# Optimization experiments

Hardware: AMD Instinct MI355X
Metric: run time of the kernel (lower is better)

Reference implementation:

```python
import jax, jax.numpy as jnp
import numpy as np

N_NODES = 100000
N_EDGES = 500000
HEADS = 4
HID = 64
N_GRAPHS = 512
EPS_SM = 1e-8
EPS_BN = 1e-5


def setup_inputs() -> dict:
    key = jax.random.key(0)
    ks = jax.random.split(key, 8)
    x = jax.random.normal(ks[0], (N_NODES, HID), dtype=jnp.float32)
    edge_index = jax.random.randint(ks[1], (2, N_EDGES), 0, N_NODES, dtype=jnp.int64)
    batch = jnp.sort(jax.random.randint(ks[2], (N_NODES,), 0, N_GRAPHS, dtype=jnp.int64))
    Ws = jax.random.normal(ks[3], (3, HEADS * HID, HID), dtype=jnp.float32) * 0.08
    att_src = jax.random.normal(ks[4], (3, HEADS, HID), dtype=jnp.float32) * 0.1
    att_dst = jax.random.normal(ks[5], (3, HEADS, HID), dtype=jnp.float32) * 0.1
    bn_gamma = jnp.ones((2, HID), dtype=jnp.float32)
    bn_beta = jnp.zeros((2, HID), dtype=jnp.float32)
    bn_mean = jnp.zeros((2, HID), dtype=jnp.float32)
    bn_var = jnp.ones((2, HID), dtype=jnp.float32)
    fc_w = jax.random.normal(ks[6], (2, HID), dtype=jnp.float32) * 0.1
    fc_b = jnp.zeros((2,), dtype=jnp.float32)
    return {"x": x, "edge_index": edge_index, "batch": batch, "Ws": Ws,
            "att_src": att_src, "att_dst": att_dst, "bn_gamma": bn_gamma,
            "bn_beta": bn_beta, "bn_mean": bn_mean, "bn_var": bn_var,
            "fc_w": fc_w, "fc_b": fc_b}


def gat_layer(x, row, col, W, a_src, a_dst):
    # x: [N, F] -> h: [N, H, C]
    n = x.shape[0]
    h = (x @ W.T).reshape(n, HEADS, HID)
    a_s = jnp.sum(h * a_src[None], axis=-1)          # [N, H]
    a_d = jnp.sum(h * a_dst[None], axis=-1)          # [N, H]
    e = a_s[row] + a_d[col]                          # [E, H]
    e = jnp.where(e >= 0, e, 0.2 * e)                # LeakyReLU(0.2)
    # segment softmax over destination node (col)
    e_max = jax.ops.segment_max(e, col, num_segments=n)  # [N, H]
    p = jnp.exp(e - e_max[col])
    p_sum = jax.ops.segment_sum(p, col, num_segments=n)
    alpha = p / (p_sum[col] + EPS_SM)                # [E, H]
    msg = h[row] * alpha[:, :, None]                 # [E, H, C]
    out = jax.ops.segment_sum(msg, col, num_segments=n)  # [N, H, C]
    return out.mean(axis=1)                          # [N, C]


def reference(x, edge_index, batch, Ws, att_src, att_dst,
              bn_gamma, bn_beta, bn_mean, bn_var, fc_w, fc_b):
    row, col = edge_index[0], edge_index[1]
    h = x
    for i in range(2):  # first num_layers-1 layers: conv -> BN(eval) -> ReLU
        h = gat_layer(h, row, col, Ws[i], att_src[i], att_dst[i])
        h = (h - bn_mean[i]) * jax.lax.rsqrt(bn_var[i] + EPS_BN) * bn_gamma[i] + bn_beta[i]
        h = jax.nn.relu(h)
        # dropout is inactive in eval mode
    h = gat_layer(h, row, col, Ws[2], att_src[2], att_dst[2])
    # global mean pool over graphs in batch
    sums = jax.ops.segment_sum(h, batch, num_segments=N_GRAPHS)          # [G, C]
    cnts = jax.ops.segment_sum(jnp.ones_like(batch, dtype=h.dtype), batch,
                               num_segments=N_GRAPHS)                    # [G]
    pooled = sums / jnp.maximum(cnts, 1.0)[:, None]
    return pooled @ fc_w.T + fc_b                                        # [G, out]
```

## Files before the change

### kernel.cpp

```cpp
#include <hip/hip_runtime.h>


#define THREADS 256
#define LDP 36

__global__ __launch_bounds__(THREADS) void k_prep(
    const float* __restrict__ Ws, const float* __restrict__ att_src,
    const float* __restrict__ att_dst, float* __restrict__ fold)
{
    int idx = blockIdx.x * THREADS + threadIdx.x;
    if (idx >= 3 * 2 * 4 * 64) return;
    int k = idx & 63, head = (idx >> 6) & 3, sd = (idx >> 8) & 1, l = idx >> 9;
    const float* att = (sd ? att_dst : att_src) + l * 256 + head * 64;
    const float* Wb  = Ws + (size_t)l * 16384 + (size_t)head * 64 * 64;
    float s = 0.f;
    #pragma unroll
    for (int c = 0; c < 64; ++c) s = fmaf(Wb[(size_t)c * 64 + k], att[c], s);
    fold[((l * 2 + sd) * 4 + head) * 64 + k] = s;
}

__global__ __launch_bounds__(THREADS) void k_gemm(
    const float* __restrict__ x, const float* __restrict__ W,
    float* __restrict__ h, int n)
{
    __shared__ float xs[128][LDP];
    __shared__ float ws[128][LDP];
    const int tid  = threadIdx.x;
    const int tc   = tid & 15;
    const int tr   = tid >> 4;
    const int row0 = blockIdx.x * 128;
    const int col0 = blockIdx.y * 128;

    float acc[8][8];
    #pragma unroll
    for (int i = 0; i < 8; ++i)
        #pragma unroll
        for (int j = 0; j < 8; ++j) acc[i][j] = 0.f;

    for (int ks2 = 0; ks2 < 2; ++ks2) {
        #pragma unroll
        for (int i = 0; i < 4; ++i) {
            int flat4 = i * 256 + tid;
            int r  = flat4 >> 3;
            int c4 = flat4 & 7;
            int gr = row0 + r;
            float4 v = make_float4(0.f, 0.f, 0.f, 0.f);
            if (gr < n) v = *(const float4*)(x + (size_t)gr * 64 + ks2 * 32 + c4 * 4);
            *(float4*)&xs[r][c4 * 4] = v;
            float4 wv = *(const float4*)(W + (size_t)(col0 + r) * 64 + ks2 * 32 + c4 * 4);
            *(float4*)&ws[r][c4 * 4] = wv;
        }
        __syncthreads();

        #pragma unroll 1
        for (int ks = 0; ks < 8; ++ks) {
            float4 xr[8];
            #pragma unroll
            for (int i = 0; i < 8; ++i) xr[i] = *(const float4*)&xs[tr + 16 * i][ks * 4];
            #pragma unroll
            for (int j = 0; j < 8; ++j) {
                float4 w4 = *(const float4*)&ws[tc + 16 * j][ks * 4];
                #pragma unroll
                for (int i = 0; i < 8; ++i) {
                    acc[i][j] = fmaf(xr[i].x, w4.x, acc[i][j]);
                    acc[i][j] = fmaf(xr[i].y, w4.y, acc[i][j]);
                    acc[i][j] = fmaf(xr[i].z, w4.z, acc[i][j]);
                    acc[i][j] = fmaf(xr[i].w, w4.w, acc[i][j]);
                }
            }
        }
        __syncthreads();
    }

    #pragma unroll
    for (int i = 0; i < 8; ++i) {
        int r = row0 + tr + 16 * i;
        if (r < n) {
            float* hp = h + (size_t)r * 256 + col0 + tc;
            #pragma unroll
            for (int j = 0; j < 8; ++j) hp[16 * j] = acc[i][j];
        }
    }
}

__global__ __launch_bounds__(THREADS) void k_att(
    const float* __restrict__ x, const float* __restrict__ fold_l,
    float* __restrict__ a_s, float* __restrict__ a_d, int n)
{
    int wid  = (blockIdx.x * THREADS + threadIdx.x) >> 6;
    int lane = threadIdx.x & 63;
    if (wid >= n) return;
    int vec = lane >> 3, ch = lane & 7;
    const float* xp = x + (size_t)wid * 64 + ch * 8;
    float4 v0 = *(const float4*)xp;
    float4 v1 = *(const float4*)(xp + 4);
    const float* fp = fold_l + vec * 64 + ch * 8;
    float acc = v0.x * fp[0] + v0.y * fp[1] + v0.z * fp[2] + v0.w * fp[3]
              + v1.x * fp[4] + v1.y * fp[5] + v1.z * fp[6] + v1.w * fp[7];
    acc += __shfl_xor(acc, 1, 64);
    acc += __shfl_xor(acc, 2, 64);
    acc += __shfl_xor(acc, 4, 64);
    if (ch == 0) {
        if (vec < 4) a_s[(size_t)wid * 4 + vec] = acc;
        else         a_d[(size_t)wid * 4 + (vec - 4)] = acc;
    }
}

__global__ __launch_bounds__(THREADS) void k_hist(
    const int* __restrict__ col, int* __restrict__ hist, int E)
{
    int e = blockIdx.x * THREADS + threadIdx.x;
    if (e < E) atomicAdd(hist + col[e], 1);
}

__global__ __launch_bounds__(THREADS) void k_scan1(
    const int* __restrict__ hist, int* __restrict__ offs, int* __restrict__ partials, int n)
{
    __shared__ int buf0[256], buf1[256];
    int tid = threadIdx.x;
    int i = blockIdx.x * 256 + tid;
    int v = (i < n) ? hist[i] : 0;
    buf0[tid] = v;
    __syncthreads();
    int* src = buf0; int* dst = buf1;
    #pragma unroll
    for (int off = 1; off < 256; off <<= 1) {
        int t = src[tid];
        if (tid >= off) t += src[tid - off];
        dst[tid] = t;
        __syncthreads();
        int* tmp = src; src = dst; dst = tmp;
    }
    if (i < n) offs[i] = src[tid] - v;
    if (tid == 255) partials[blockIdx.x] = src[255];
}

__global__ __launch_bounds__(512) void k_scan2(int* __restrict__ partials, int nb)
{
    __shared__ int buf0[512], buf1[512];
    int tid = threadIdx.x;
    int v = (tid < nb) ? partials[tid] : 0;
    buf0[tid] = v;
    __syncthreads();
    int* src = buf0; int* dst = buf1;
    #pragma unroll
    for (int off = 1; off < 512; off <<= 1) {
        int t = src[tid];
        if (tid >= off) t += src[tid - off];
        dst[tid] = t;
        __syncthreads();
        int* tmp = src; src = dst; dst = tmp;
    }
    if (tid < nb) partials[tid] = src[tid] - v;
}

__global__ __launch_bounds__(THREADS) void k_scan3(
    int* __restrict__ offs, const int* __restrict__ partials, int n)
{
    int i = blockIdx.x * THREADS + threadIdx.x;
    if (i < n) offs[i] += partials[i >> 8];
}

__global__ __launch_bounds__(THREADS) void k_scatter(
    const int* __restrict__ row, const int* __restrict__ col,
    const int* __restrict__ offs, int* __restrict__ tmpc,
    int* __restrict__ rs, int E)
{
    int e = blockIdx.x * THREADS + threadIdx.x;
    if (e >= E) return;
    int c = col[e];
    int pos = offs[c] + atomicAdd(tmpc + c, 1);
    rs[pos] = row[e];
}

__global__ __launch_bounds__(THREADS) void k_alpha(
    const int* __restrict__ rs, const int* __restrict__ offs, const int* __restrict__ deg,
    const float* __restrict__ a_s, const float* __restrict__ a_d,
    float* __restrict__ alpha, int n)
{
    int v = blockIdx.x * THREADS + threadIdx.x;
    if (v >= n) return;
    const int start = offs[v];
    const int d     = deg[v];
    const float4 ad = *(const float4*)(a_d + (size_t)v * 4);

    float m0 = -1e30f, m1 = -1e30f, m2 = -1e30f, m3 = -1e30f;
    for (int i = 0; i < d; ++i) {
        int r = rs[start + i];
        float4 as = *(const float4*)(a_s + (size_t)r * 4);
        float v0 = as.x + ad.x, v1 = as.y + ad.y, v2 = as.z + ad.z, v3 = as.w + ad.w;
        v0 = v0 >= 0.f ? v0 : 0.2f * v0;
        v1 = v1 >= 0.f ? v1 : 0.2f * v1;
        v2 = v2 >= 0.f ? v2 : 0.2f * v2;
        v3 = v3 >= 0.f ? v3 : 0.2f * v3;
        *(float4*)(alpha + (size_t)(start + i) * 4) = make_float4(v0, v1, v2, v3);
        m0 = fmaxf(m0, v0); m1 = fmaxf(m1, v1); m2 = fmaxf(m2, v2); m3 = fmaxf(m3, v3);
    }
    float ps0 = 0.f, ps1 = 0.f, ps2 = 0.f, ps3 = 0.f;
    for (int i = 0; i < d; ++i) {
        float4 s = *(const float4*)(alpha + (size_t)(start + i) * 4);
        float p0 = __expf(s.x - m0), p1 = __expf(s.y - m1);
        float p2 = __expf(s.z - m2), p3 = __expf(s.w - m3);
        ps0 += p0; ps1 += p1; ps2 += p2; ps3 += p3;
        *(float4*)(alpha + (size_t)(start + i) * 4) = make_float4(p0, p1, p2, p3);
    }
    float i0 = 0.25f / (ps0 + 1e-8f), i1 = 0.25f / (ps1 + 1e-8f);
    float i2 = 0.25f / (ps2 + 1e-8f), i3 = 0.25f / (ps3 + 1e-8f);
    for (int i = 0; i < d; ++i) {
        float4 s = *(const float4*)(alpha + (size_t)(start + i) * 4);
        *(float4*)(alpha + (size_t)(start + i) * 4) =
            make_float4(s.x * i0, s.y * i1, s.z * i2, s.w * i3);
    }
}

__global__ __launch_bounds__(THREADS) void k_gat(
    const int* __restrict__ rs, const int* __restrict__ offs, const int* __restrict__ deg,
    const float* __restrict__ alpha, const float* __restrict__ h,
    const float* __restrict__ bng, const float* __restrict__ bnb,
    const float* __restrict__ bnm, const float* __restrict__ bnv, int use_bn,
    float* __restrict__ out, int n)
{
    int wid  = (blockIdx.x * THREADS + threadIdx.x) >> 6;
    int lane = threadIdx.x & 63;
    if (wid >= n) return;
    const int start = offs[wid];
    const int d     = deg[wid];

    float acc = 0.f;
    for (int i = 0; i < d; ++i) {
        int r = rs[start + i];
        float4 a = *(const float4*)(alpha + (size_t)(start + i) * 4);
        const float* hb = h + (size_t)r * 256;
        acc = fmaf(a.x, hb[lane],       acc);
        acc = fmaf(a.y, hb[64 + lane],  acc);
        acc = fmaf(a.z, hb[128 + lane], acc);
        acc = fmaf(a.w, hb[192 + lane], acc);
    }
    if (use_bn) {
        float scale = bng[lane] * rsqrtf(bnv[lane] + 1e-5f);
        float shift = bnb[lane] - bnm[lane] * scale;
        acc = fmaxf(fmaf(acc, scale, shift), 0.f);
    }
    out[(size_t)wid * 64 + lane] = acc;
}

#define POOL_CHUNK 32
__global__ __launch_bounds__(THREADS) void k_pool(
    const float* __restrict__ xf, const int* __restrict__ batch,
    float* __restrict__ sums, float* __restrict__ cnt, int n)
{
    int wid  = (blockIdx.x * THREADS + threadIdx.x) >> 6;
    int lane = threadIdx.x & 63;
    int n0 = wid * POOL_CHUNK;
    if (n0 >= n) return;
    int n1 = min(n0 + POOL_CHUNK, n);
    int g = batch[n0];
    float acc = 0.f, c = 0.f;
    for (int i = n0; i < n1; ++i) {
        int gi = batch[i];
        if (gi != g) {
            atomicAdd(sums + (size_t)g * 64 + lane, acc);
            if (lane == 0) atomicAdd(cnt + g, c);
            g = gi; acc = 0.f; c = 0.f;
        }
        acc += xf[(size_t)i * 64 + lane];
        c += 1.f;
    }
    atomicAdd(sums + (size_t)g * 64 + lane, acc);
    if (lane == 0) atomicAdd(cnt + g, c);
}

__global__ __launch_bounds__(THREADS) void k_fc(
    const float* __restrict__ sums, const float* __restrict__ cnt,
    const float* __restrict__ fw, const float* __restrict__ fb,
    float* __restrict__ out, int G)
{
    int g = blockIdx.x * THREADS + threadIdx.x;
    if (g >= G) return;
    float cdiv = fmaxf(cnt[g], 1.f);
    float o0 = fb[0], o1 = fb[1];
    for (int k = 0; k < 64; ++k) {
        float p = sums[(size_t)g * 64 + k] / cdiv;
        o0 = fmaf(p, fw[k], o0);
        o1 = fmaf(p, fw[64 + k], o1);
    }
    out[(size_t)g * 2 + 0] = o0;
    out[(size_t)g * 2 + 1] = o1;
}

static inline size_t align256(size_t x) { return (x + 255) & ~(size_t)255; }

extern "C" void kernel_launch(void* const* d_in, const int* in_sizes, int n_in,
                              void* d_out, int out_size, void* d_ws, size_t ws_size,
                              hipStream_t stream)
{
    const float* x        = (const float*)d_in[0];
    const int*   eidx     = (const int*)d_in[1];
    const int*   batch    = (const int*)d_in[2];
    const float* Ws       = (const float*)d_in[3];
    const float* att_src  = (const float*)d_in[4];
    const float* att_dst  = (const float*)d_in[5];
    const float* bn_gamma = (const float*)d_in[6];
    const float* bn_beta  = (const float*)d_in[7];
    const float* bn_mean  = (const float*)d_in[8];
    const float* bn_var   = (const float*)d_in[9];
    const float* fc_w     = (const float*)d_in[10];
    const float* fc_b     = (const float*)d_in[11];

    const int N = in_sizes[0] / 64;
    const int E = in_sizes[1] / 2;
    const int G = 512;
    const int* row = eidx;
    const int* col = eidx + E;

    char* p = (char*)d_ws;
    float* h     = (float*)p; p += align256((size_t)N * 256 * 4);
    float* a_s   = (float*)p; p += align256((size_t)N * 4 * 4);
    float* a_d   = (float*)p; p += align256((size_t)N * 4 * 4);
    float* xb0   = (float*)p; p += align256((size_t)N * 64 * 4);
    float* xb1   = (float*)p; p += align256((size_t)N * 64 * 4);
    int*   hist  = (int*)p;   p += align256((size_t)N * 4);
    int*   offs  = (int*)p;   p += align256((size_t)N * 4);
    int*   tmpc  = (int*)p;   p += align256((size_t)N * 4);
    int*   part  = (int*)p;   p += align256((size_t)1024 * 4);
    int*   rs    = (int*)p;   p += align256((size_t)E * 4);
    float* alpha = (float*)p; p += align256((size_t)E * 4 * 4);
    float* fold  = (float*)p; p += align256((size_t)1536 * 4);
    float* sums  = (float*)p; p += align256((size_t)G * 64 * 4);
    float* cnt   = (float*)p; p += align256((size_t)G * 4);
    (void)ws_size; (void)n_in; (void)out_size;

    const int nb = (N + 255) / 256;

    k_prep<<<6, THREADS, 0, stream>>>(Ws, att_src, att_dst, fold);
    hipMemsetAsync(hist, 0, (size_t)N * 4, stream);
    hipMemsetAsync(tmpc, 0, (size_t)N * 4, stream);
    k_hist<<<(E + THREADS - 1) / THREADS, THREADS, 0, stream>>>(col, hist, E);
    k_scan1<<<nb, THREADS, 0, stream>>>(hist, offs, part, N);
    k_scan2<<<1, 512, 0, stream>>>(part, nb);
    k_scan3<<<nb, THREADS, 0, stream>>>(offs, part, N);
    k_scatter<<<(E + THREADS - 1) / THREADS, THREADS, 0, stream>>>(row, col, offs, tmpc, rs, E);

    const float* xin = x;
    for (int l = 0; l < 3; ++l) {
        float* xout = (l == 1) ? xb1 : xb0;
        dim3 ggrid((N + 127) / 128, 2);
        k_gemm<<<ggrid, THREADS, 0, stream>>>(xin, Ws + (size_t)l * 16384, h, N);
        k_att<<<((size_t)N * 64 + THREADS - 1) / THREADS, THREADS, 0, stream>>>(
            xin, fold + (size_t)l * 512, a_s, a_d, N);
        k_alpha<<<(N + THREADS - 1) / THREADS, THREADS, 0, stream>>>(
            rs, offs, hist, a_s, a_d, alpha, N);
        k_gat<<<((size_t)N * 64 + THREADS - 1) / THREADS, THREADS, 0, stream>>>(
            rs, offs, hist, alpha, h,
            bn_gamma + l * 64, bn_beta + l * 64, bn_mean + l * 64, bn_var + l * 64,
            (l < 2) ? 1 : 0, xout, N);
        xin = xout;
    }

    hipMemsetAsync(sums, 0, (size_t)G * 64 * 4, stream);
    hipMemsetAsync(cnt, 0, (size_t)G * 4, stream);
    int pool_waves = (N + POOL_CHUNK - 1) / POOL_CHUNK;
    k_pool<<<((size_t)pool_waves * 64 + THREADS - 1) / THREADS, THREADS, 0, stream>>>(
        xin, batch, sums, cnt, N);
    k_fc<<<(G + THREADS - 1) / THREADS, THREADS, 0, stream>>>(
        sums, cnt, fc_w, fc_b, (float*)d_out, G);
}
```

Baseline: 630.9 us.

## Interleave head columns in h and defer softmax normalization to aggregation

The GEMM now permutes W's output rows so that h is stored with the four heads interleaved per channel. Each lane in the aggregation kernel can then load one float4 per neighbor instead of four strided scalars. The softmax normalization pass in k_alpha is removed: per-node sums are written to a new psum buffer, and k_gat applies the reciprocal scale inline. This drops a full read-write pass over alpha, at the cost of extra multiplies in the gather loop and a small extra buffer.

```diff
diff --git a/kernel.cpp b/kernel.cpp
--- a/kernel.cpp
+++ b/kernel.cpp
@@ -47,7 +47,9 @@
             float4 v = make_float4(0.f, 0.f, 0.f, 0.f);
             if (gr < n) v = *(const float4*)(x + (size_t)gr * 64 + ks2 * 32 + c4 * 4);
             *(float4*)&xs[r][c4 * 4] = v;
-            float4 wv = *(const float4*)(W + (size_t)(col0 + r) * 64 + ks2 * 32 + c4 * 4);
+            int gp = col0 + r;
+            int pr = (gp & 3) * 64 + (gp >> 2);
+            float4 wv = *(const float4*)(W + (size_t)pr * 64 + ks2 * 32 + c4 * 4);
             *(float4*)&ws[r][c4 * 4] = wv;
         }
         __syncthreads();
@@ -176,7 +178,7 @@
 __global__ __launch_bounds__(THREADS) void k_alpha(
     const int* __restrict__ rs, const int* __restrict__ offs, const int* __restrict__ deg,
     const float* __restrict__ a_s, const float* __restrict__ a_d,
-    float* __restrict__ alpha, int n)
+    float* __restrict__ alpha, float* __restrict__ psum, int n)
 {
     int v = blockIdx.x * THREADS + threadIdx.x;
     if (v >= n) return;
@@ -204,18 +206,13 @@
         ps0 += p0; ps1 += p1; ps2 += p2; ps3 += p3;
         *(float4*)(alpha + (size_t)(start + i) * 4) = make_float4(p0, p1, p2, p3);
     }
-    float i0 = 0.25f / (ps0 + 1e-8f), i1 = 0.25f / (ps1 + 1e-8f);
-    float i2 = 0.25f / (ps2 + 1e-8f), i3 = 0.25f / (ps3 + 1e-8f);
-    for (int i = 0; i < d; ++i) {
-        float4 s = *(const float4*)(alpha + (size_t)(start + i) * 4);
-        *(float4*)(alpha + (size_t)(start + i) * 4) =
-            make_float4(s.x * i0, s.y * i1, s.z * i2, s.w * i3);
-    }
+    *(float4*)(psum + (size_t)v * 4) = make_float4(ps0, ps1, ps2, ps3);
 }
 
 __global__ __launch_bounds__(THREADS) void k_gat(
     const int* __restrict__ rs, const int* __restrict__ offs, const int* __restrict__ deg,
-    const float* __restrict__ alpha, const float* __restrict__ h,
+    const float* __restrict__ alpha, const float* __restrict__ psum,
+    const float* __restrict__ h,
     const float* __restrict__ bng, const float* __restrict__ bnb,
     const float* __restrict__ bnm, const float* __restrict__ bnv, int use_bn,
     float* __restrict__ out, int n)
@@ -225,16 +222,19 @@
     if (wid >= n) return;
     const int start = offs[wid];
     const int d     = deg[wid];
+    float4 ps = *(const float4*)(psum + (size_t)wid * 4);
+    const float i0 = 0.25f / (ps.x + 1e-8f), i1 = 0.25f / (ps.y + 1e-8f);
+    const float i2 = 0.25f / (ps.z + 1e-8f), i3 = 0.25f / (ps.w + 1e-8f);
 
     float acc = 0.f;
     for (int i = 0; i < d; ++i) {
         int r = rs[start + i];
         float4 a = *(const float4*)(alpha + (size_t)(start + i) * 4);
-        const float* hb = h + (size_t)r * 256;
-        acc = fmaf(a.x, hb[lane],       acc);
-        acc = fmaf(a.y, hb[64 + lane],  acc);
-        acc = fmaf(a.z, hb[128 + lane], acc);
-        acc = fmaf(a.w, hb[192 + lane], acc);
+        float4 v = *(const float4*)(h + (size_t)r * 256 + lane * 4);
+        acc = fmaf(a.x * i0, v.x, acc);
+        acc = fmaf(a.y * i1, v.y, acc);
+        acc = fmaf(a.z * i2, v.z, acc);
+        acc = fmaf(a.w * i3, v.w, acc);
     }
     if (use_bn) {
         float scale = bng[lane] * rsqrtf(bnv[lane] + 1e-5f);
@@ -317,6 +317,7 @@
     float* h     = (float*)p; p += align256((size_t)N * 256 * 4);
     float* a_s   = (float*)p; p += align256((size_t)N * 4 * 4);
     float* a_d   = (float*)p; p += align256((size_t)N * 4 * 4);
+    float* psum  = (float*)p; p += align256((size_t)N * 4 * 4);
     float* xb0   = (float*)p; p += align256((size_t)N * 64 * 4);
     float* xb1   = (float*)p; p += align256((size_t)N * 64 * 4);
     int*   hist  = (int*)p;   p += align256((size_t)N * 4);
@@ -349,9 +350,9 @@
         k_att<<<((size_t)N * 64 + THREADS - 1) / THREADS, THREADS, 0, stream>>>(
             xin, fold + (size_t)l * 512, a_s, a_d, N);
         k_alpha<<<(N + THREADS - 1) / THREADS, THREADS, 0, stream>>>(
-            rs, offs, hist, a_s, a_d, alpha, N);
+            rs, offs, hist, a_s, a_d, alpha, psum, N);
         k_gat<<<((size_t)N * 64 + THREADS - 1) / THREADS, THREADS, 0, stream>>>(
-            rs, offs, hist, alpha, h,
+            rs, offs, hist, alpha, psum, h,
             bn_gamma + l * 64, bn_beta + l * 64, bn_mean + l * 64, bn_var + l * 64,
             (l < 2) ? 1 : 0, xout, N);
         xin = xout;
```

Measured after the change: 611.2 us. 1.03x faster.
